# Optimization experiments

Measured on AMD Instinct MI355X. Metric: run time of the kernel, lower is better.

The kernel has to match this reference:

```python
import jax, jax.numpy as jnp
import numpy as np

N_HEADS = 12
NEG_INF = -1e9


def rotate_half(x):
    x1, x2 = jnp.split(x, 2, axis=-1)
    return jnp.concatenate((-x2, x1), axis=-1)


def rope_tables(T, D, dtype):
    # matches RotaryEmbedding buffers: emb = cat(freqs, freqs), shape [1,1,T,D]
    inv_freq = 1.0 / (10000.0 ** (jnp.arange(0, D, 2, dtype=jnp.float32) / D))
    t = jnp.arange(T, dtype=jnp.float32)
    freqs = jnp.einsum('i,j->ij', t, inv_freq)
    emb = jnp.concatenate((freqs, freqs), axis=-1)
    return jnp.cos(emb)[None, None].astype(dtype), jnp.sin(emb)[None, None].astype(dtype)


def setup_inputs() -> dict:
    key = jax.random.key(0)
    ks = jax.random.split(key, 5)
    B, T, C = 4, 2048, 768
    s = 1.0 / np.sqrt(C)
    x = jax.random.normal(ks[0], (B, T, C), dtype=jnp.float32)
    wq = jax.random.normal(ks[1], (C, C), dtype=jnp.float32) * s
    wk = jax.random.normal(ks[2], (C, C), dtype=jnp.float32) * s
    wv = jax.random.normal(ks[3], (C, C), dtype=jnp.float32) * s
    wo = jax.random.normal(ks[4], (C, C), dtype=jnp.float32) * s
    causal = jnp.tril(jnp.ones((T, T), dtype=bool))
    mask = jnp.where(causal, 0.0, NEG_INF).astype(jnp.float32)[None, None]
    return {"x": x, "wq": wq, "wk": wk, "wv": wv, "wo": wo, "mask": mask}


def reference(x, wq, wk, wv, wo, mask):
    B, T, C = x.shape
    H = N_HEADS
    D = C // H
    # QKV projections (no bias), reshape to [B,H,T,D]
    def proj(w):
        return (x @ w).reshape(B, T, H, D).transpose(0, 2, 1, 3)
    q, k, v = proj(wq), proj(wk), proj(wv)
    cos, sin = rope_tables(T, D, x.dtype)
    q = q * cos + rotate_half(q) * sin
    k = k * cos + rotate_half(k) * sin
    attn = jnp.einsum('bhqd,bhkd->bhqk', q, k) / jnp.sqrt(jnp.asarray(D, x.dtype))
    attn = attn + mask
    attn = jax.nn.softmax(attn, axis=-1)  # dropout = identity (eval mode)
    out = jnp.einsum('bhqk,bhkd->bhqd', attn, v)
    out = out.transpose(0, 2, 1, 3).reshape(B, T, C)
    return out @ wo
```

## Files before the change

kernel.cpp:

```cpp
#include <hip/hip_runtime.h>
#include <hip/hip_bf16.h>
#include <cmath>

typedef _Float16 f16x8 __attribute__((ext_vector_type(8)));
typedef float f32x4 __attribute__((ext_vector_type(4)));

#define T_SEQ 2048
#define C_DIM 768
#define H_NUM 12
#define NX (8192 * 768)
#define NW (768 * 768)

__device__ __forceinline__ unsigned short f2h(float f) {
    _Float16 h = (_Float16)f;
    return __builtin_bit_cast(unsigned short, h);
}

__device__ __forceinline__ float fexp2(float x) {
#if __has_builtin(__builtin_amdgcn_exp2f)
    return __builtin_amdgcn_exp2f(x);
#else
    return exp2f(x);
#endif
}

__device__ __forceinline__ unsigned int pkrtz(float a, float b) {
    auto r = __builtin_amdgcn_cvt_pkrtz(a, b);
    return __builtin_bit_cast(unsigned int, r);
}

__device__ __forceinline__ unsigned int permlo(unsigned int d0, unsigned int d1) {
#if __has_builtin(__builtin_amdgcn_perm)
    return __builtin_amdgcn_perm(d1, d0, 0x05040100u);
#else
    return (d0 & 0xffffu) | (d1 << 16);
#endif
}
__device__ __forceinline__ unsigned int permhi(unsigned int d0, unsigned int d1) {
#if __has_builtin(__builtin_amdgcn_perm)
    return __builtin_amdgcn_perm(d1, d0, 0x07060302u);
#else
    return (d0 >> 16) | (d1 & 0xffff0000u);
#endif
}

__device__ __forceinline__ void gld16(const unsigned short* g, unsigned short* l) {
    __builtin_amdgcn_global_load_lds(
        (const __attribute__((address_space(1))) unsigned int*)g,
        (__attribute__((address_space(3))) unsigned int*)l, 16, 0, 0);
}

__global__ __launch_bounds__(256)
void prep(const float* __restrict__ x,
          const float* __restrict__ w0, const float* __restrict__ w1,
          const float* __restrict__ w2, const float* __restrict__ w3,
          unsigned short* __restrict__ xb, unsigned short* __restrict__ wt) {
    __shared__ float T[64][65];
    const int pid = blockIdx.x;
    if (pid < 3072) {
        int cidx = pid * 256 + threadIdx.x;
        int row = cidx / 96;
        int cp = cidx - row * 96;
        int dchunk = row * 96 + (cp & ~3) + ((cp & 3) ^ (row & 3));
        const float* s = x + (size_t)cidx * 8;
        float4 v0 = *(const float4*)s, v1 = *(const float4*)(s + 4);
        ushort4 a, b;
        a.x = f2h(v0.x); a.y = f2h(v0.y); a.z = f2h(v0.z); a.w = f2h(v0.w);
        b.x = f2h(v1.x); b.y = f2h(v1.y); b.z = f2h(v1.z); b.w = f2h(v1.w);
        unsigned short* d = xb + (size_t)dchunk * 8;
        *(ushort4*)d = a;
        *(ushort4*)(d + 4) = b;
    } else {
        int t = pid - 3072;
        int z = t / 144, r = t - z * 144;
        int kx = r / 12, ny = r - kx * 12;
        const float* src = (z == 0) ? w0 : (z == 1) ? w1 : (z == 2) ? w2 : w3;
        unsigned short* dst = wt + (size_t)z * NW;
        const int k0 = kx * 64, n0 = ny * 64;
        const int tid = threadIdx.x;
        {
            int rowb = tid >> 4, c4 = (tid & 15) * 4;
#pragma unroll
            for (int i = 0; i < 4; ++i) {
                int row = rowb + i * 16;
                float4 v = *(const float4*)&src[(size_t)(k0 + row) * C_DIM + n0 + c4];
                T[row][c4] = v.x; T[row][c4 + 1] = v.y; T[row][c4 + 2] = v.z; T[row][c4 + 3] = v.w;
            }
        }
        __syncthreads();
        {
            int n = tid & 63, kseg = (tid >> 6) * 16;
            int n_glob = n0 + n;
            unsigned short tmp[16];
#pragma unroll
            for (int j = 0; j < 16; ++j) tmp[j] = f2h(T[kseg + j][n]);
            int base = k0 + (kseg & 32);
            int sub = (kseg >> 3) & 3;
            unsigned short* drow = dst + (size_t)n_glob * C_DIM + base;
            *(uint4*)&drow[(sub ^ (n_glob & 3)) << 3]       = *(uint4*)&tmp[0];
            *(uint4*)&drow[((sub + 1) ^ (n_glob & 3)) << 3] = *(uint4*)&tmp[8];
        }
    }
}

__global__ __launch_bounds__(256, 3)
void qkv_gemm(const unsigned short* __restrict__ xb,
              const unsigned short* __restrict__ wt,
              unsigned short* __restrict__ q_ws,
              unsigned short* __restrict__ k_ws,
              unsigned short* __restrict__ vt_ws) {
    const int pid = blockIdx.x;
    const int xcd = pid & 7, idx = pid >> 3;
    const int mloc = idx / 18, nw = idx - mloc * 18;
    const int which = nw % 3, nx = nw / 3;
    const unsigned short* W = wt + (size_t)which * NW;
    const int n0 = nx * 128, m0 = (xcd * 8 + mloc) * 128;

    __shared__ __align__(16) unsigned short As[2 * 128 * 32];
    __shared__ __align__(16) unsigned short Bs[2 * 128 * 32];

    const int tid = threadIdx.x, lane = tid & 63, w = tid >> 6;
    const int quad = lane >> 4, l16 = lane & 15;
    const int wm = (w >> 1) * 64, wn = (w & 1) * 64;

    f32x4 acc[4][4] = {};

    for (int k0 = 0; k0 < C_DIM; k0 += 64) {
        __syncthreads();
#pragma unroll
        for (int c = 0; c < 4; ++c) {
            int e = c * 256 + tid;
            int p = e >> 9, row = (e >> 2) & 127, ch = e & 3;
            int kc = k0 + p * 32 + ch * 8;
            gld16(xb + (size_t)(m0 + row) * C_DIM + kc, &As[e * 8]);
            gld16(W  + (size_t)(n0 + row) * C_DIM + kc, &Bs[e * 8]);
        }
        __syncthreads();
#pragma unroll
        for (int p = 0; p < 2; ++p) {
            f16x8 af[4], bf[4];
#pragma unroll
            for (int mt = 0; mt < 4; ++mt) {
                int r = wm + mt * 16 + l16;
                af[mt] = *(const f16x8*)&As[p * 4096 + r * 32 + ((quad ^ (r & 3)) << 3)];
            }
#pragma unroll
            for (int nt = 0; nt < 4; ++nt) {
                int r = wn + nt * 16 + l16;
                bf[nt] = *(const f16x8*)&Bs[p * 4096 + r * 32 + ((quad ^ (r & 3)) << 3)];
            }
#pragma unroll
            for (int mt = 0; mt < 4; ++mt)
#pragma unroll
                for (int nt = 0; nt < 4; ++nt)
                    acc[mt][nt] = __builtin_amdgcn_mfma_f32_16x16x32_f16(af[mt], bf[nt], acc[mt][nt], 0, 0, 0);
        }
    }

    const int head = nx * 2 + (w & 1);

    if (which < 2) {
        unsigned short* dst = (which == 0) ? q_ws : k_ws;
        const float qscale = 0.18033688011112042f;
#pragma unroll
        for (int ntp = 0; ntp < 2; ++ntp) {
            int d1 = ntp * 16 + l16;
            float invf = __expf(-0.28782313662425572f * (float)d1);
#pragma unroll
            for (int mt = 0; mt < 4; ++mt)
#pragma unroll
                for (int reg = 0; reg < 4; ++reg) {
                    int m = m0 + wm + mt * 16 + quad * 4 + reg;
                    int t = m & (T_SEQ - 1), bb = m >> 11;
                    float sn, cs;
                    __sincosf((float)t * invf, &sn, &cs);
                    float v1 = acc[mt][ntp][reg], v2 = acc[mt][ntp + 2][reg];
                    float o1 = v1 * cs - v2 * sn;
                    float o2 = v2 * cs + v1 * sn;
                    if (which == 0) { o1 *= qscale; o2 *= qscale; }
                    size_t o = ((size_t)(bb * H_NUM + head) * T_SEQ + t) * 64 + d1;
                    dst[o] = f2h(o1);
                    dst[o + 32] = f2h(o2);
                }
        }
    } else {
#pragma unroll
        for (int nt = 0; nt < 4; ++nt) {
            int d = nt * 16 + l16;
#pragma unroll
            for (int mt = 0; mt < 4; ++mt) {
                int m = m0 + wm + mt * 16 + quad * 4;
                int t = m & (T_SEQ - 1), bb = m >> 11;
                ushort4 pk;
                pk.x = f2h(acc[mt][nt][0]); pk.y = f2h(acc[mt][nt][1]);
                pk.z = f2h(acc[mt][nt][2]); pk.w = f2h(acc[mt][nt][3]);
                *(ushort4*)&vt_ws[((size_t)(bb * H_NUM + head) * 64 + d) * T_SEQ + t] = pk;
            }
        }
    }
}

__global__ __launch_bounds__(256, 3)
void flash_attn(const unsigned short* __restrict__ q_ws,
                const unsigned short* __restrict__ k_ws,
                const unsigned short* __restrict__ vt_ws,
                unsigned short* __restrict__ attn_out) {
    __shared__ __align__(16) unsigned short Kbuf[2][64 * 64];
    __shared__ __align__(16) unsigned short Vbuf[2][64 * 64];
    __shared__ __align__(16) unsigned int Ps32[4][16 * 64];

    const int pid = blockIdx.x;
    const int xcd = pid & 7, slot = pid >> 3;
    const int bh = xcd * 6 + (slot >> 4);
    const int pr = slot & 15;
    const int qa = pr, qb = 31 - pr;
    const int b = bh / H_NUM, h = bh % H_NUM;

    const int tid = threadIdx.x, lane = tid & 63, w = tid >> 6;
    const int quad = lane >> 4, l16 = lane & 15;
    const size_t base = (size_t)bh * (T_SEQ * 64);

    const unsigned short* qAp = q_ws + base + (size_t)(qa * 64 + w * 16 + l16) * 64 + quad * 8;
    f16x8 aqA0 = *(const f16x8*)(qAp);
    f16x8 aqA1 = *(const f16x8*)(qAp + 32);
    const unsigned short* qBp = q_ws + base + (size_t)(qb * 64 + w * 16 + l16) * 64 + quad * 8;
    f16x8 aqB0 = *(const f16x8*)(qBp);
    f16x8 aqB1 = *(const f16x8*)(qBp + 32);

    f32x4 accA[4] = {}, accB[4] = {};
    float lA[4] = {}, lB[4] = {};
    unsigned int* pw = &Ps32[w][0];

    const int r_in = lane >> 3;
    const int cpr = lane & 7;
    const int gch = (cpr ^ r_in) * 8;

#define DMA_KV(P, KT)                                                                  \
    {                                                                                  \
        _Pragma("unroll")                                                              \
        for (int j = 0; j < 2; ++j) {                                                  \
            int row = w * 16 + j * 8 + r_in;                                           \
            gld16(k_ws + base + (size_t)((KT) * 64 + row) * 64 + gch,                  \
                  &Kbuf[P][(w * 16 + j * 8) * 64]);                                    \
            gld16(vt_ws + base + (size_t)row * T_SEQ + (KT) * 64 + gch,                \
                  &Vbuf[P][(w * 16 + j * 8) * 64]);                                    \
        }                                                                              \
    }

    const int fo = (quad ^ (l16 & 7)) << 3;

    const int rbit = (l16 >> 2) & 1;
    const int rp0 = l16 * 64 + ((quad * 8 + 16 * rbit) & 63);
    const int rp1 = l16 * 64 + (((32 + quad * 8) + 16 * rbit) & 63);
    const int wbase = (quad * 4) * 64;
    const int wcol0 = ((l16 + 16 * (quad & 1)) & 63);

    DMA_KV(0, 0);
    for (int kt = 0; kt <= qb; ++kt) {
        const int cur = kt & 1;
        __syncthreads();
        if (kt < qb) DMA_KV(cur ^ 1, kt + 1);
        const int doA = (kt <= qa);

        f16x8 bk[4][2], bv[4][2];
#pragma unroll
        for (int nt = 0; nt < 4; ++nt) {
            const unsigned short* kr = &Kbuf[cur][(nt * 16 + l16) * 64 + fo];
            bk[nt][0] = *(const f16x8*)(kr);
            bk[nt][1] = *(const f16x8*)((const unsigned short*)((size_t)kr ^ 64));
            const unsigned short* vr = &Vbuf[cur][(nt * 16 + l16) * 64 + fo];
            bv[nt][0] = *(const f16x8*)(vr);
            bv[nt][1] = *(const f16x8*)((const unsigned short*)((size_t)vr ^ 64));
        }

        f32x4 sB[4] = {}, sA[4] = {};
#pragma unroll
        for (int nt = 0; nt < 4; ++nt) {
            sB[nt] = __builtin_amdgcn_mfma_f32_16x16x32_f16(aqB0, bk[nt][0], sB[nt], 0, 0, 0);
            sB[nt] = __builtin_amdgcn_mfma_f32_16x16x32_f16(aqB1, bk[nt][1], sB[nt], 0, 0, 0);
        }
        if (doA) {
#pragma unroll
            for (int nt = 0; nt < 4; ++nt) {
                sA[nt] = __builtin_amdgcn_mfma_f32_16x16x32_f16(aqA0, bk[nt][0], sA[nt], 0, 0, 0);
                sA[nt] = __builtin_amdgcn_mfma_f32_16x16x32_f16(aqA1, bk[nt][1], sA[nt], 0, 0, 0);
            }
        }
        if (kt == qb) {
#pragma unroll
            for (int nt = 0; nt < 4; ++nt)
#pragma unroll
                for (int reg = 0; reg < 4; ++reg)
                    if (nt * 16 + l16 > w * 16 + quad * 4 + reg) sB[nt][reg] = -1e30f;
        }
        if (kt == qa) {
#pragma unroll
            for (int nt = 0; nt < 4; ++nt)
#pragma unroll
                for (int reg = 0; reg < 4; ++reg)
                    if (nt * 16 + l16 > w * 16 + quad * 4 + reg) sA[nt][reg] = -1e30f;
        }

        if (doA) {
#pragma unroll
            for (int nt = 0; nt < 4; ++nt)
#pragma unroll
                for (int reg = 0; reg < 4; ++reg) {
                    float pB = fexp2(fminf(sB[nt][reg], 15.0f));
                    float pA = fexp2(fminf(sA[nt][reg], 15.0f));
                    lB[reg] += pB;
                    lA[reg] += pA;
                    pw[(wbase + reg * 64) + ((wcol0 + nt * 16) & 63)] = pkrtz(pB, pA);
                }
        } else {
#pragma unroll
            for (int nt = 0; nt < 4; ++nt)
#pragma unroll
                for (int reg = 0; reg < 4; ++reg) {
                    float pB = fexp2(fminf(sB[nt][reg], 15.0f));
                    lB[reg] += pB;
                    pw[(wbase + reg * 64) + ((wcol0 + nt * 16) & 63)] = pkrtz(pB, pB);
                }
        }

        uint4 c0 = *(const uint4*)(pw + rp0);
        uint4 c1 = *(const uint4*)(pw + rp0 + 4);
        uint4 c2 = *(const uint4*)(pw + rp1);
        uint4 c3 = *(const uint4*)(pw + rp1 + 4);

        uint4 lo0 = { permlo(c0.x, c0.y), permlo(c0.z, c0.w), permlo(c1.x, c1.y), permlo(c1.z, c1.w) };
        uint4 lo1 = { permlo(c2.x, c2.y), permlo(c2.z, c2.w), permlo(c3.x, c3.y), permlo(c3.z, c3.w) };
        f16x8 apB0 = __builtin_bit_cast(f16x8, lo0);
        f16x8 apB1 = __builtin_bit_cast(f16x8, lo1);
#pragma unroll
        for (int nt = 0; nt < 4; ++nt) {
            accB[nt] = __builtin_amdgcn_mfma_f32_16x16x32_f16(apB0, bv[nt][0], accB[nt], 0, 0, 0);
            accB[nt] = __builtin_amdgcn_mfma_f32_16x16x32_f16(apB1, bv[nt][1], accB[nt], 0, 0, 0);
        }
        if (doA) {
            uint4 hi0 = { permhi(c0.x, c0.y), permhi(c0.z, c0.w), permhi(c1.x, c1.y), permhi(c1.z, c1.w) };
            uint4 hi1 = { permhi(c2.x, c2.y), permhi(c2.z, c2.w), permhi(c3.x, c3.y), permhi(c3.z, c3.w) };
            f16x8 apA0 = __builtin_bit_cast(f16x8, hi0);
            f16x8 apA1 = __builtin_bit_cast(f16x8, hi1);
#pragma unroll
            for (int nt = 0; nt < 4; ++nt) {
                accA[nt] = __builtin_amdgcn_mfma_f32_16x16x32_f16(apA0, bv[nt][0], accA[nt], 0, 0, 0);
                accA[nt] = __builtin_amdgcn_mfma_f32_16x16x32_f16(apA1, bv[nt][1], accA[nt], 0, 0, 0);
            }
        }
    }
#undef DMA_KV

#pragma unroll
    for (int reg = 0; reg < 4; ++reg) {
        float v = lB[reg];
        v += __shfl_xor(v, 1); v += __shfl_xor(v, 2);
        v += __shfl_xor(v, 4); v += __shfl_xor(v, 8);
        lB[reg] = 1.0f / v;
        float u = lA[reg];
        u += __shfl_xor(u, 1); u += __shfl_xor(u, 2);
        u += __shfl_xor(u, 4); u += __shfl_xor(u, 8);
        lA[reg] = 1.0f / u;
    }
#pragma unroll
    for (int nt = 0; nt < 4; ++nt)
#pragma unroll
        for (int reg = 0; reg < 4; ++reg) {
            int col = h * 64 + nt * 16 + l16;
            int tB = qb * 64 + w * 16 + quad * 4 + reg;
            attn_out[(size_t)(b * T_SEQ + tB) * C_DIM + col] = f2h(accB[nt][reg] * lB[reg]);
            int tA = qa * 64 + w * 16 + quad * 4 + reg;
            attn_out[(size_t)(b * T_SEQ + tA) * C_DIM + col] = f2h(accA[nt][reg] * lA[reg]);
        }
}

__global__ __launch_bounds__(256, 3)
void out_proj(const unsigned short* __restrict__ ab,
              const unsigned short* __restrict__ wt_o,
              float* __restrict__ out) {
    const int pid = blockIdx.x;
    const int xcd = pid & 7, idx = pid >> 3;
    const int mloc = idx / 6, nx = idx - mloc * 6;
    const int n0 = nx * 128, m0 = (xcd * 8 + mloc) * 128;

    __shared__ __align__(16) unsigned short As[2 * 128 * 32];
    __shared__ __align__(16) unsigned short Bs[2 * 128 * 32];

    const int tid = threadIdx.x, lane = tid & 63, w = tid >> 6;
    const int quad = lane >> 4, l16 = lane & 15;
    const int wm = (w >> 1) * 64, wn = (w & 1) * 64;

    f32x4 acc[4][4] = {};
    const int srow = tid >> 1, shalf = tid & 1;

    for (int k0 = 0; k0 < C_DIM; k0 += 64) {
        __syncthreads();
#pragma unroll
        for (int p = 0; p < 2; ++p) {
            const unsigned short* g = ab + (size_t)(m0 + srow) * C_DIM + k0 + p * 32 + shalf * 16;
            uint4 d0 = *(const uint4*)g;
            uint4 d1 = *(const uint4*)(g + 8);
            *(uint4*)&As[p * 4096 + srow * 32 + (((shalf * 2 + 0) ^ (srow & 3)) << 3)] = d0;
            *(uint4*)&As[p * 4096 + srow * 32 + (((shalf * 2 + 1) ^ (srow & 3)) << 3)] = d1;
        }
#pragma unroll
        for (int c = 0; c < 4; ++c) {
            int e = c * 256 + tid;
            int p = e >> 9, row = (e >> 2) & 127, ch = e & 3;
            gld16(wt_o + (size_t)(n0 + row) * C_DIM + k0 + p * 32 + ch * 8, &Bs[e * 8]);
        }
        __syncthreads();
#pragma unroll
        for (int p = 0; p < 2; ++p) {
            f16x8 af[4], bf[4];
#pragma unroll
            for (int mt = 0; mt < 4; ++mt) {
                int r = wm + mt * 16 + l16;
                af[mt] = *(const f16x8*)&As[p * 4096 + r * 32 + ((quad ^ (r & 3)) << 3)];
            }
#pragma unroll
            for (int nt = 0; nt < 4; ++nt) {
                int r = wn + nt * 16 + l16;
                bf[nt] = *(const f16x8*)&Bs[p * 4096 + r * 32 + ((quad ^ (r & 3)) << 3)];
            }
#pragma unroll
            for (int mt = 0; mt < 4; ++mt)
#pragma unroll
                for (int nt = 0; nt < 4; ++nt)
                    acc[mt][nt] = __builtin_amdgcn_mfma_f32_16x16x32_f16(af[mt], bf[nt], acc[mt][nt], 0, 0, 0);
        }
    }

#pragma unroll
    for (int mt = 0; mt < 4; ++mt)
#pragma unroll
        for (int nt = 0; nt < 4; ++nt)
#pragma unroll
            for (int reg = 0; reg < 4; ++reg) {
                int m = m0 + wm + mt * 16 + quad * 4 + reg;
                int n = n0 + wn + nt * 16 + l16;
                out[(size_t)m * C_DIM + n] = acc[mt][nt][reg];
            }
}

extern "C" void kernel_launch(void* const* d_in, const int* in_sizes, int n_in,
                              void* d_out, int out_size, void* d_ws, size_t ws_size,
                              hipStream_t stream) {
    const float* x  = (const float*)d_in[0];
    const float* wq = (const float*)d_in[1];
    const float* wk = (const float*)d_in[2];
    const float* wv = (const float*)d_in[3];
    const float* wo = (const float*)d_in[4];
    float* out = (float*)d_out;

    unsigned short* xb    = (unsigned short*)d_ws;
    unsigned short* wt    = xb + NX;
    unsigned short* q_ws  = wt + 4 * (size_t)NW;
    unsigned short* k_ws  = q_ws + NX;
    unsigned short* vt_ws = k_ws + NX;
    unsigned short* attn  = xb;

    prep<<<3648, 256, 0, stream>>>(x, wq, wk, wv, wo, xb, wt);
    qkv_gemm<<<1152, 256, 0, stream>>>(xb, wt, q_ws, k_ws, vt_ws);
    flash_attn<<<768, 256, 0, stream>>>(q_ws, k_ws, vt_ws, attn);
    out_proj<<<384, 256, 0, stream>>>(attn, wt + 3 * (size_t)NW, out);
}
```

Baseline: 224.3 us.

## Double-buffer LDS in QKV and output GEMMs; reswizzle attention P-tile layout

The QKV and output-projection GEMMs now keep two LDS buffers per operand. Each iteration prefetches the next K-slice while computing on the current one, which drops one barrier per iteration and overlaps global loads with MFMA work. Doubling LDS use lowers the launch-bounds occupancy target from 3 to 2 blocks per CU. Separately, the attention kernel's P-matrix LDS write/read addressing gets a new XOR swizzle, meant to cut bank conflicts on the transposing round-trip.

```diff
diff --git a/kernel.cpp b/kernel.cpp
--- a/kernel.cpp
+++ b/kernel.cpp
@@ -103,7 +103,7 @@
     }
 }
 
-__global__ __launch_bounds__(256, 3)
+__global__ __launch_bounds__(256, 2)
 void qkv_gemm(const unsigned short* __restrict__ xb,
               const unsigned short* __restrict__ wt,
               unsigned short* __restrict__ q_ws,
@@ -116,8 +116,8 @@
     const unsigned short* W = wt + (size_t)which * NW;
     const int n0 = nx * 128, m0 = (xcd * 8 + mloc) * 128;
 
-    __shared__ __align__(16) unsigned short As[2 * 128 * 32];
-    __shared__ __align__(16) unsigned short Bs[2 * 128 * 32];
+    __shared__ __align__(16) unsigned short As[2 * 8192];
+    __shared__ __align__(16) unsigned short Bs[2 * 8192];
 
     const int tid = threadIdx.x, lane = tid & 63, w = tid >> 6;
     const int quad = lane >> 4, l16 = lane & 15;
@@ -125,29 +125,35 @@
 
     f32x4 acc[4][4] = {};
 
-    for (int k0 = 0; k0 < C_DIM; k0 += 64) {
+#define STAGE(BUF, K0)                                                              \
+    {                                                                               \
+        _Pragma("unroll")                                                           \
+        for (int c = 0; c < 4; ++c) {                                               \
+            int e = c * 256 + tid;                                                  \
+            int p = e >> 9, row = (e >> 2) & 127, ch = e & 3;                       \
+            int kc = (K0) + p * 32 + ch * 8;                                        \
+            gld16(xb + (size_t)(m0 + row) * C_DIM + kc, &As[(BUF) * 8192 + e * 8]); \
+            gld16(W  + (size_t)(n0 + row) * C_DIM + kc, &Bs[(BUF) * 8192 + e * 8]); \
+        }                                                                           \
+    }
+
+    STAGE(0, 0)
+    for (int kk = 0; kk < 12; ++kk) {
+        const int cur = kk & 1;
         __syncthreads();
-#pragma unroll
-        for (int c = 0; c < 4; ++c) {
-            int e = c * 256 + tid;
-            int p = e >> 9, row = (e >> 2) & 127, ch = e & 3;
-            int kc = k0 + p * 32 + ch * 8;
-            gld16(xb + (size_t)(m0 + row) * C_DIM + kc, &As[e * 8]);
-            gld16(W  + (size_t)(n0 + row) * C_DIM + kc, &Bs[e * 8]);
-        }
-        __syncthreads();
+        if (kk < 11) STAGE(cur ^ 1, (kk + 1) * 64)
 #pragma unroll
         for (int p = 0; p < 2; ++p) {
             f16x8 af[4], bf[4];
 #pragma unroll
             for (int mt = 0; mt < 4; ++mt) {
                 int r = wm + mt * 16 + l16;
-                af[mt] = *(const f16x8*)&As[p * 4096 + r * 32 + ((quad ^ (r & 3)) << 3)];
+                af[mt] = *(const f16x8*)&As[cur * 8192 + p * 4096 + r * 32 + ((quad ^ (r & 3)) << 3)];
             }
 #pragma unroll
             for (int nt = 0; nt < 4; ++nt) {
                 int r = wn + nt * 16 + l16;
-                bf[nt] = *(const f16x8*)&Bs[p * 4096 + r * 32 + ((quad ^ (r & 3)) << 3)];
+                bf[nt] = *(const f16x8*)&Bs[cur * 8192 + p * 4096 + r * 32 + ((quad ^ (r & 3)) << 3)];
             }
 #pragma unroll
             for (int mt = 0; mt < 4; ++mt)
@@ -156,6 +162,7 @@
                     acc[mt][nt] = __builtin_amdgcn_mfma_f32_16x16x32_f16(af[mt], bf[nt], acc[mt][nt], 0, 0, 0);
         }
     }
+#undef STAGE
 
     const int head = nx * 2 + (w & 1);
 
@@ -249,11 +256,12 @@
 
     const int fo = (quad ^ (l16 & 7)) << 3;
 
-    const int rbit = (l16 >> 2) & 1;
-    const int rp0 = l16 * 64 + ((quad * 8 + 16 * rbit) & 63);
-    const int rp1 = l16 * 64 + (((32 + quad * 8) + 16 * rbit) & 63);
-    const int wbase = (quad * 4) * 64;
-    const int wcol0 = ((l16 + 16 * (quad & 1)) & 63);
+    const int wg = (quad & 1) * 4;
+    const int l16q = l16 >> 2, l16m = l16 & 3;
+    const int s7 = l16 & 7;
+    const int rA = l16 * 64;
+    const int rp0a = rA + (((2 * quad) ^ s7) << 2);
+    const int rp0b = rA + (((2 * quad + 1) ^ s7) << 2);
 
     DMA_KV(0, 0);
     for (int kt = 0; kt <= qb; ++kt) {
@@ -310,7 +318,7 @@
                     float pA = fexp2(fminf(sA[nt][reg], 15.0f));
                     lB[reg] += pB;
                     lA[reg] += pA;
-                    pw[(wbase + reg * 64) + ((wcol0 + nt * 16) & 63)] = pkrtz(pB, pA);
+                    pw[(quad * 4 + reg) * 64 + ((((nt * 4) | l16q) ^ (wg | reg)) << 2) + l16m] = pkrtz(pB, pA);
                 }
         } else {
 #pragma unroll
@@ -319,14 +327,14 @@
                 for (int reg = 0; reg < 4; ++reg) {
                     float pB = fexp2(fminf(sB[nt][reg], 15.0f));
                     lB[reg] += pB;
-                    pw[(wbase + reg * 64) + ((wcol0 + nt * 16) & 63)] = pkrtz(pB, pB);
+                    pw[(quad * 4 + reg) * 64 + ((((nt * 4) | l16q) ^ (wg | reg)) << 2) + l16m] = pkrtz(pB, pB);
                 }
         }
 
-        uint4 c0 = *(const uint4*)(pw + rp0);
-        uint4 c1 = *(const uint4*)(pw + rp0 + 4);
-        uint4 c2 = *(const uint4*)(pw + rp1);
-        uint4 c3 = *(const uint4*)(pw + rp1 + 4);
+        uint4 c0 = *(const uint4*)(pw + rp0a);
+        uint4 c1 = *(const uint4*)(pw + rp0b);
+        uint4 c2 = *(const uint4*)(pw + rp0a + 32);
+        uint4 c3 = *(const uint4*)(pw + rp0b + 32);
 
         uint4 lo0 = { permlo(c0.x, c0.y), permlo(c0.z, c0.w), permlo(c1.x, c1.y), permlo(c1.z, c1.w) };
         uint4 lo1 = { permlo(c2.x, c2.y), permlo(c2.z, c2.w), permlo(c3.x, c3.y), permlo(c3.z, c3.w) };
@@ -374,7 +382,7 @@
         }
 }
 
-__global__ __launch_bounds__(256, 3)
+__global__ __launch_bounds__(256, 2)
 void out_proj(const unsigned short* __restrict__ ab,
               const unsigned short* __restrict__ wt_o,
               float* __restrict__ out) {
@@ -383,8 +391,8 @@
     const int mloc = idx / 6, nx = idx - mloc * 6;
     const int n0 = nx * 128, m0 = (xcd * 8 + mloc) * 128;
 
-    __shared__ __align__(16) unsigned short As[2 * 128 * 32];
-    __shared__ __align__(16) unsigned short Bs[2 * 128 * 32];
+    __shared__ __align__(16) unsigned short As[2 * 8192];
+    __shared__ __align__(16) unsigned short Bs[2 * 8192];
 
     const int tid = threadIdx.x, lane = tid & 63, w = tid >> 6;
     const int quad = lane >> 4, l16 = lane & 15;
@@ -393,35 +401,53 @@
     f32x4 acc[4][4] = {};
     const int srow = tid >> 1, shalf = tid & 1;
 
-    for (int k0 = 0; k0 < C_DIM; k0 += 64) {
+#define STAGE_B(BUF, K0)                                                                  \
+    {                                                                                     \
+        _Pragma("unroll")                                                                 \
+        for (int c = 0; c < 4; ++c) {                                                     \
+            int e = c * 256 + tid;                                                        \
+            int p = e >> 9, row = (e >> 2) & 127, ch = e & 3;                             \
+            gld16(wt_o + (size_t)(n0 + row) * C_DIM + (K0) + p * 32 + ch * 8,             \
+                  &Bs[(BUF) * 8192 + e * 8]);                                             \
+        }                                                                                 \
+    }
+#define STAGE_A(BUF, K0)                                                                  \
+    {                                                                                     \
+        uint4 d0[2], d1[2];                                                               \
+        _Pragma("unroll")                                                                 \
+        for (int p = 0; p < 2; ++p) {                                                     \
+            const unsigned short* g = ab + (size_t)(m0 + srow) * C_DIM + (K0) + p * 32 + shalf * 16; \
+            d0[p] = *(const uint4*)g;                                                     \
+            d1[p] = *(const uint4*)(g + 8);                                               \
+        }                                                                                 \
+        _Pragma("unroll")                                                                 \
+        for (int p = 0; p < 2; ++p) {                                                     \
+            *(uint4*)&As[(BUF) * 8192 + p * 4096 + srow * 32 + (((shalf * 2 + 0) ^ (srow & 3)) << 3)] = d0[p]; \
+            *(uint4*)&As[(BUF) * 8192 + p * 4096 + srow * 32 + (((shalf * 2 + 1) ^ (srow & 3)) << 3)] = d1[p]; \
+        }                                                                                 \
+    }
+
+    STAGE_A(0, 0)
+    STAGE_B(0, 0)
+    for (int kk = 0; kk < 12; ++kk) {
+        const int cur = kk & 1;
         __syncthreads();
-#pragma unroll
-        for (int p = 0; p < 2; ++p) {
-            const unsigned short* g = ab + (size_t)(m0 + srow) * C_DIM + k0 + p * 32 + shalf * 16;
-            uint4 d0 = *(const uint4*)g;
-            uint4 d1 = *(const uint4*)(g + 8);
-            *(uint4*)&As[p * 4096 + srow * 32 + (((shalf * 2 + 0) ^ (srow & 3)) << 3)] = d0;
-            *(uint4*)&As[p * 4096 + srow * 32 + (((shalf * 2 + 1) ^ (srow & 3)) << 3)] = d1;
-        }
-#pragma unroll
-        for (int c = 0; c < 4; ++c) {
-            int e = c * 256 + tid;
-            int p = e >> 9, row = (e >> 2) & 127, ch = e & 3;
-            gld16(wt_o + (size_t)(n0 + row) * C_DIM + k0 + p * 32 + ch * 8, &Bs[e * 8]);
-        }
-        __syncthreads();
+        if (kk < 11) {
+            STAGE_A(cur ^ 1, (kk + 1) * 64)
+            STAGE_B(cur ^ 1, (kk + 1) * 64)
+        }
 #pragma unroll
         for (int p = 0; p < 2; ++p) {
             f16x8 af[4], bf[4];
 #pragma unroll
             for (int mt = 0; mt < 4; ++mt) {
                 int r = wm + mt * 16 + l16;
-                af[mt] = *(const f16x8*)&As[p * 4096 + r * 32 + ((quad ^ (r & 3)) << 3)];
+                af[mt] = *(const f16x8*)&As[cur * 8192 + p * 4096 + r * 32 + ((quad ^ (r & 3)) << 3)];
             }
 #pragma unroll
             for (int nt = 0; nt < 4; ++nt) {
                 int r = wn + nt * 16 + l16;
-                bf[nt] = *(const f16x8*)&Bs[p * 4096 + r * 32 + ((quad ^ (r & 3)) << 3)];
+                bf[nt] = *(const f16x8*)&Bs[cur * 8192 + p * 4096 + r * 32 + ((quad ^ (r & 3)) << 3)];
             }
 #pragma unroll
             for (int mt = 0; mt < 4; ++mt)
@@ -430,6 +456,8 @@
                     acc[mt][nt] = __builtin_amdgcn_mfma_f32_16x16x32_f16(af[mt], bf[nt], acc[mt][nt], 0, 0, 0);
         }
     }
+#undef STAGE_A
+#undef STAGE_B
 
 #pragma unroll
     for (int mt = 0; mt < 4; ++mt)
```

After: 235.7 us. 5.1% more time.

## Compute softmax row sums via MFMA with ones and reswizzle P scratch

Applied to the files above, without the earlier changes.

Replaces the per-lane scalar accumulation of softmax denominators and the final cross-lane shuffle reduction with extra MFMA ops that multiply the fp16 P tile by a ones vector. The denominator then comes from the same rounded P values used in the PV product. The change also drops the fminf clamp before exp2, switches the P shared-memory write/read layout to an XOR swizzle meant to cut bank conflicts, and raises the qkv_gemm occupancy hint from 3 to 4. Risks include overflow without the clamp and register pressure under the higher occupancy bound.

```diff
diff --git a/kernel.cpp b/kernel.cpp
--- a/kernel.cpp
+++ b/kernel.cpp
@@ -103,7 +103,7 @@
     }
 }
 
-__global__ __launch_bounds__(256, 3)
+__global__ __launch_bounds__(256, 4)
 void qkv_gemm(const unsigned short* __restrict__ xb,
               const unsigned short* __restrict__ wt,
               unsigned short* __restrict__ q_ws,
@@ -116,8 +116,8 @@
     const unsigned short* W = wt + (size_t)which * NW;
     const int n0 = nx * 128, m0 = (xcd * 8 + mloc) * 128;
 
-    __shared__ __align__(16) unsigned short As[2 * 128 * 32];
-    __shared__ __align__(16) unsigned short Bs[2 * 128 * 32];
+    __shared__ __align__(16) unsigned short As[8192];
+    __shared__ __align__(16) unsigned short Bs[8192];
 
     const int tid = threadIdx.x, lane = tid & 63, w = tid >> 6;
     const int quad = lane >> 4, l16 = lane & 15;
@@ -228,7 +228,11 @@
     f16x8 aqB1 = *(const f16x8*)(qBp + 32);
 
     f32x4 accA[4] = {}, accB[4] = {};
-    float lA[4] = {}, lB[4] = {};
+    f32x4 laccA = {}, laccB = {};
+    f16x8 onesf;
+#pragma unroll
+    for (int i = 0; i < 8; ++i) onesf[i] = (_Float16)1.0f;
+
     unsigned int* pw = &Ps32[w][0];
 
     const int r_in = lane >> 3;
@@ -249,11 +253,12 @@
 
     const int fo = (quad ^ (l16 & 7)) << 3;
 
-    const int rbit = (l16 >> 2) & 1;
-    const int rp0 = l16 * 64 + ((quad * 8 + 16 * rbit) & 63);
-    const int rp1 = l16 * 64 + (((32 + quad * 8) + 16 * rbit) & 63);
-    const int wbase = (quad * 4) * 64;
-    const int wcol0 = ((l16 + 16 * (quad & 1)) & 63);
+    const int wg = (quad & 1) * 4;
+    const int l16q = l16 >> 2, l16m = l16 & 3;
+    const int s7 = l16 & 7;
+    const int rA = l16 * 64;
+    const int rp0a = rA + (((2 * quad) ^ s7) << 2);
+    const int rp0b = rA + (((2 * quad + 1) ^ s7) << 2);
 
     DMA_KV(0, 0);
     for (int kt = 0; kt <= qb; ++kt) {
@@ -306,27 +311,24 @@
             for (int nt = 0; nt < 4; ++nt)
 #pragma unroll
                 for (int reg = 0; reg < 4; ++reg) {
-                    float pB = fexp2(fminf(sB[nt][reg], 15.0f));
-                    float pA = fexp2(fminf(sA[nt][reg], 15.0f));
-                    lB[reg] += pB;
-                    lA[reg] += pA;
-                    pw[(wbase + reg * 64) + ((wcol0 + nt * 16) & 63)] = pkrtz(pB, pA);
+                    float pB = fexp2(sB[nt][reg]);
+                    float pA = fexp2(sA[nt][reg]);
+                    pw[(quad * 4 + reg) * 64 + ((((nt * 4) | l16q) ^ (wg | reg)) << 2) + l16m] = pkrtz(pB, pA);
                 }
         } else {
 #pragma unroll
             for (int nt = 0; nt < 4; ++nt)
 #pragma unroll
                 for (int reg = 0; reg < 4; ++reg) {
-                    float pB = fexp2(fminf(sB[nt][reg], 15.0f));
-                    lB[reg] += pB;
-                    pw[(wbase + reg * 64) + ((wcol0 + nt * 16) & 63)] = pkrtz(pB, pB);
+                    float pB = fexp2(sB[nt][reg]);
+                    pw[(quad * 4 + reg) * 64 + ((((nt * 4) | l16q) ^ (wg | reg)) << 2) + l16m] = pkrtz(pB, pB);
                 }
         }
 
-        uint4 c0 = *(const uint4*)(pw + rp0);
-        uint4 c1 = *(const uint4*)(pw + rp0 + 4);
-        uint4 c2 = *(const uint4*)(pw + rp1);
-        uint4 c3 = *(const uint4*)(pw + rp1 + 4);
+        uint4 c0 = *(const uint4*)(pw + rp0a);
+        uint4 c1 = *(const uint4*)(pw + rp0b);
+        uint4 c2 = *(const uint4*)(pw + rp0a + 32);
+        uint4 c3 = *(const uint4*)(pw + rp0b + 32);
 
         uint4 lo0 = { permlo(c0.x, c0.y), permlo(c0.z, c0.w), permlo(c1.x, c1.y), permlo(c1.z, c1.w) };
         uint4 lo1 = { permlo(c2.x, c2.y), permlo(c2.z, c2.w), permlo(c3.x, c3.y), permlo(c3.z, c3.w) };
@@ -337,6 +339,8 @@
             accB[nt] = __builtin_amdgcn_mfma_f32_16x16x32_f16(apB0, bv[nt][0], accB[nt], 0, 0, 0);
             accB[nt] = __builtin_amdgcn_mfma_f32_16x16x32_f16(apB1, bv[nt][1], accB[nt], 0, 0, 0);
         }
+        laccB = __builtin_amdgcn_mfma_f32_16x16x32_f16(apB0, onesf, laccB, 0, 0, 0);
+        laccB = __builtin_amdgcn_mfma_f32_16x16x32_f16(apB1, onesf, laccB, 0, 0, 0);
         if (doA) {
             uint4 hi0 = { permhi(c0.x, c0.y), permhi(c0.z, c0.w), permhi(c1.x, c1.y), permhi(c1.z, c1.w) };
             uint4 hi1 = { permhi(c2.x, c2.y), permhi(c2.z, c2.w), permhi(c3.x, c3.y), permhi(c3.z, c3.w) };
@@ -347,20 +351,17 @@
                 accA[nt] = __builtin_amdgcn_mfma_f32_16x16x32_f16(apA0, bv[nt][0], accA[nt], 0, 0, 0);
                 accA[nt] = __builtin_amdgcn_mfma_f32_16x16x32_f16(apA1, bv[nt][1], accA[nt], 0, 0, 0);
             }
+            laccA = __builtin_amdgcn_mfma_f32_16x16x32_f16(apA0, onesf, laccA, 0, 0, 0);
+            laccA = __builtin_amdgcn_mfma_f32_16x16x32_f16(apA1, onesf, laccA, 0, 0, 0);
         }
     }
 #undef DMA_KV
 
+    float lB[4], lA[4];
 #pragma unroll
     for (int reg = 0; reg < 4; ++reg) {
-        float v = lB[reg];
-        v += __shfl_xor(v, 1); v += __shfl_xor(v, 2);
-        v += __shfl_xor(v, 4); v += __shfl_xor(v, 8);
-        lB[reg] = 1.0f / v;
-        float u = lA[reg];
-        u += __shfl_xor(u, 1); u += __shfl_xor(u, 2);
-        u += __shfl_xor(u, 4); u += __shfl_xor(u, 8);
-        lA[reg] = 1.0f / u;
+        lB[reg] = 1.0f / laccB[reg];
+        lA[reg] = 1.0f / laccA[reg];
     }
 #pragma unroll
     for (int nt = 0; nt < 4; ++nt)
@@ -383,8 +384,8 @@
     const int mloc = idx / 6, nx = idx - mloc * 6;
     const int n0 = nx * 128, m0 = (xcd * 8 + mloc) * 128;
 
-    __shared__ __align__(16) unsigned short As[2 * 128 * 32];
-    __shared__ __align__(16) unsigned short Bs[2 * 128 * 32];
+    __shared__ __align__(16) unsigned short As[8192];
+    __shared__ __align__(16) unsigned short Bs[8192];
 
     const int tid = threadIdx.x, lane = tid & 63, w = tid >> 6;
     const int quad = lane >> 4, l16 = lane & 15;
```

After: 219.5 us. -2.2%, faster.
